# Performance work log

Measured on AMD Instinct MI355X. Metric: run time of the kernel, lower is better.

## Reference

```python
import jax, jax.numpy as jnp
import numpy as np
import math

N_EMBD = 1024
N_HEAD = 16
HEAD_DIM = N_EMBD // N_HEAD


def setup_inputs() -> dict:
    key = jax.random.key(0)
    k_x, k_w1, k_b1, k_w2, k_b2 = jax.random.split(key, 5)
    B, T = 2, 2048
    x = jax.random.normal(k_x, (B, T, N_EMBD), dtype=jnp.float32)
    # ln1: Linear(n_embd, 3*n_embd); weights stored as [in, out] for x @ W
    W_qkv = jax.random.normal(k_w1, (N_EMBD, 3 * N_EMBD), dtype=jnp.float32) * 0.02
    b_qkv = jax.random.normal(k_b1, (3 * N_EMBD,), dtype=jnp.float32) * 0.02
    # ln2: Linear(n_embd, n_embd)
    W_out = jax.random.normal(k_w2, (N_EMBD, N_EMBD), dtype=jnp.float32) * 0.02
    b_out = jax.random.normal(k_b2, (N_EMBD,), dtype=jnp.float32) * 0.02
    return {"x": x, "W_qkv": W_qkv, "b_qkv": b_qkv, "W_out": W_out, "b_out": b_out}


def reference(x, W_qkv, b_qkv, W_out, b_out):
    B, T, C = x.shape
    qkv = x @ W_qkv + b_qkv                      # [B,T,3C]
    q, k, v = jnp.split(qkv, 3, axis=-1)
    # reshape to heads: [B, H, T, D]
    def to_heads(t):
        return t.reshape(B, T, N_HEAD, HEAD_DIM).transpose(0, 2, 1, 3)
    Q, K, V = to_heads(q), to_heads(k), to_heads(v)
    # NOTE: scale is 1/sqrt(n_head), as in the source (not sqrt(head_dim));
    # NOTE: no causal mask is applied, faithfully matching the source forward.
    scale = 1.0 / math.sqrt(N_HEAD)
    scores = jnp.einsum('bhqd,bhkd->bhqk', Q, K) * scale  # [B,H,T,T]
    attn = jax.nn.softmax(scores, axis=-1)
    out = jnp.einsum('bhqk,bhkd->bhqd', attn, V)          # [B,H,T,D]
    out = out.transpose(0, 2, 1, 3).reshape(B, T, C)
    # dropout = 0.0 -> identity (eval mode)
    return out @ W_out + b_out
```

## Files before the change

### kernel.cpp

```cpp
#include <hip/hip_runtime.h>
#include <hip/hip_bf16.h>
#include <stdint.h>

typedef __bf16 bf16_t;
typedef __bf16 bf16x8 __attribute__((ext_vector_type(8)));
typedef float  f32x4  __attribute__((ext_vector_type(4)));

#define AS1 __attribute__((address_space(1)))
#define AS3 __attribute__((address_space(3)))

__device__ __forceinline__ void gload16(const bf16_t* g, char* l) {
  __builtin_amdgcn_global_load_lds((AS1 const void*)(uintptr_t)g, (AS3 void*)l, 16, 0, 0);
}
__device__ __forceinline__ int swz8(int r) { return (r & 7) ^ ((r >> 2) & 6); }

#define C2S 0.36067376022224085f
#define LGKM0 do { asm volatile("s_waitcnt lgkmcnt(0)" ::: "memory"); \
                   __builtin_amdgcn_sched_barrier(0); } while (0)

__global__ __launch_bounds__(256) void prep(
    const float* __restrict__ x, const float* __restrict__ Wqkv, const float* __restrict__ Wout,
    bf16_t* __restrict__ xb, bf16_t* __restrict__ wqkvT, bf16_t* __restrict__ woutT) {
  __shared__ float tile[32][33];
  const int bid = blockIdx.x, tid = threadIdx.x;
  if (bid < 4096) {
    const int i = bid * 256 + tid;
    float4 v = reinterpret_cast<const float4*>(x)[i];
    union { bf16_t h[4]; unsigned long long u; } r;
    r.h[0] = (bf16_t)v.x; r.h[1] = (bf16_t)v.y; r.h[2] = (bf16_t)v.z; r.h[3] = (bf16_t)v.w;
    reinterpret_cast<unsigned long long*>(xb)[i] = r.u;
    return;
  }
  const float* W; bf16_t* Wt; int N, tb;
  if (bid < 7168) { W = Wqkv; Wt = wqkvT; N = 3072; tb = bid - 4096; }
  else            { W = Wout; Wt = woutT; N = 1024; tb = bid - 7168; }
  const int kb = (tb & 31) * 32, nb = (tb >> 5) * 32;
  const int tx = tid & 31, ty = tid >> 5;
#pragma unroll
  for (int i = 0; i < 32; i += 8)
    tile[ty + i][tx] = W[(size_t)(kb + ty + i) * N + nb + tx];
  __syncthreads();
#pragma unroll
  for (int i = 0; i < 32; i += 8)
    Wt[(size_t)(nb + ty + i) * 1024 + kb + tx] = (bf16_t)tile[tx][ty + i];
}

__global__ __launch_bounds__(512) void gemm8(
    const bf16_t* __restrict__ A, const bf16_t* __restrict__ Bt,
    const float* __restrict__ bias,
    bf16_t* __restrict__ outb, bf16_t* __restrict__ vtb,
    int N, int K, int ldo) {
  __shared__ bf16_t lA[3][4096];
  __shared__ bf16_t lB[3][4096];
  const int tid = threadIdx.x;
  const int wave = tid >> 6, lane = tid & 63;
  const int lr = lane & 15, lg = lane >> 4;
  const int ntiles = N >> 7;
  const int bid = (blockIdx.x & 7) * ((int)gridDim.x >> 3) + (blockIdx.x >> 3);
  const int bn = bid % ntiles, bm = bid / ntiles;
  const int m0 = bm * 128, n0 = bn * 128;
  const int wr = wave >> 2, wc = wave & 3;
  f32x4 acc[4][2] = {};

  const int srow = tid >> 2;
  const int scolb = ((tid & 3) << 4) ^ (((srow >> 1) & 3) << 4);
  const bf16_t* Asrc = A  + (size_t)(m0 + srow) * K + (scolb >> 1);
  const bf16_t* Bsrc = Bt + (size_t)(n0 + srow) * K + (scolb >> 1);
  auto stage = [&](int buf, int k0) {
    char* dst = (char*)nullptr;
    (void)dst;
    gload16(Asrc + k0, (char*)&lA[buf][0] + wave * 1024);
    gload16(Bsrc + k0, (char*)&lB[buf][0] + wave * 1024);
  };

  auto ldA = [&](const char* p, int mi) {
    const int row = wr * 64 + mi * 16 + lr;
    return *reinterpret_cast<const bf16x8*>(p + row * 64 + ((lg * 16) ^ (((row >> 1) & 3) << 4)));
  };
  auto ldB = [&](const char* p, int ni) {
    const int row = wc * 32 + ni * 16 + lr;
    return *reinterpret_cast<const bf16x8*>(p + row * 64 + ((lg * 16) ^ (((row >> 1) & 3) << 4)));
  };

  const int nt = K >> 5;
  stage(0, 0);
  stage(1, 32);
  int cur = 0, stg = 2;

  for (int t = 0; t < nt; ++t) {
    if (t + 2 < nt) {
      stage(stg, (t + 2) << 5);
      asm volatile("s_waitcnt vmcnt(4)" ::: "memory");
    } else if (t + 1 < nt) {
      asm volatile("s_waitcnt vmcnt(2)" ::: "memory");
    } else {
      asm volatile("s_waitcnt vmcnt(0)" ::: "memory");
    }
    __builtin_amdgcn_s_barrier();
    __builtin_amdgcn_sched_barrier(0);

    const char* pA = (const char*)&lA[cur][0];
    const char* pB = (const char*)&lB[cur][0];
    bf16x8 af[4], bfv[2];
#pragma unroll
    for (int mi = 0; mi < 4; ++mi) af[mi] = ldA(pA, mi);
    bfv[0] = ldB(pB, 0); bfv[1] = ldB(pB, 1);

    __builtin_amdgcn_s_setprio(1);
#pragma unroll
    for (int mi = 0; mi < 4; ++mi)
#pragma unroll
      for (int ni = 0; ni < 2; ++ni)
        acc[mi][ni] = __builtin_amdgcn_mfma_f32_16x16x32_bf16(af[mi], bfv[ni], acc[mi][ni], 0, 0, 0);
    __builtin_amdgcn_s_setprio(0);

    __builtin_amdgcn_sched_barrier(0);
    __builtin_amdgcn_s_barrier();
    cur = cur == 2 ? 0 : cur + 1;
    stg = stg == 2 ? 0 : stg + 1;
  }

#pragma unroll
  for (int mi = 0; mi < 4; ++mi) {
#pragma unroll
    for (int ni = 0; ni < 2; ++ni) {
      const int col = n0 + wc * 32 + ni * 16 + lr;
      const float bv = bias[col];
      const int rg0 = m0 + wr * 64 + mi * 16 + lg * 4;
      if (col >= 2048) {
        const int colv = col - 2048;
        const int dd = colv & 63, hh = colv >> 6;
        const int bb = rg0 >> 11, t = rg0 & 2047;
        union { bf16_t h4[4]; unsigned long long u; } pk;
#pragma unroll
        for (int r = 0; r < 4; ++r) pk.h4[r] = (bf16_t)(acc[mi][ni][r] + bv);
        *reinterpret_cast<unsigned long long*>(
            vtb + (size_t)(bb * 16 + hh) * 131072 + (size_t)dd * 2048 + t) = pk.u;
      } else {
        const float sc = (col < 1024) ? C2S : 1.f;
#pragma unroll
        for (int r = 0; r < 4; ++r) {
          const float v = (acc[mi][ni][r] + bv) * sc;
          outb[(size_t)(rg0 + r) * ldo + col] = (bf16_t)v;
        }
      }
    }
  }
}

template<int MI>
__global__ __launch_bounds__(256) void gemm_bt(
    const bf16_t* __restrict__ A, const bf16_t* __restrict__ Bt,
    const float* __restrict__ bias,
    bf16_t* __restrict__ outb, bf16_t* __restrict__ vtb, float* __restrict__ outf,
    int M, int N, int K, int ldo, int mode) {
  __shared__ bf16_t lA[3][MI * 1024];
  __shared__ bf16_t lB[3][4096];
  const int tid = threadIdx.x;
  const int wave = tid >> 6, lane = tid & 63;
  const int lr = lane & 15, lg = lane >> 4;
  const int ntiles = N >> 7;
  const int bid = (blockIdx.x & 7) * ((int)gridDim.x >> 3) + (blockIdx.x >> 3);
  const int bn = bid % ntiles, bm = bid / ntiles;
  const int m0 = bm * (MI * 32), n0 = bn * 128;
  const int wr = wave >> 1, wc = wave & 1;
  f32x4 acc[MI][4] = {};

  const int lamw = wave * 64 + lane;
  const int srow = lamw >> 2;
  const int scolb = ((lamw & 3) << 4) ^ (((srow >> 1) & 3) << 4);
  auto stageA = [&](int buf, int k0, int it) {
    gload16(A + (size_t)(m0 + it * 64 + srow) * K + k0 + (scolb >> 1),
            (char*)&lA[buf][0] + (it * 256 + wave * 64) * 16);
  };
  auto stageB = [&](int buf, int k0, int it) {
    gload16(Bt + (size_t)(n0 + it * 64 + srow) * K + k0 + (scolb >> 1),
            (char*)&lB[buf][0] + (it * 256 + wave * 64) * 16);
  };
  auto stageg = [&](int buf, int k0) {
#pragma unroll
    for (int it = 0; it < MI / 2; ++it) stageA(buf, k0, it);
    stageB(buf, k0, 0); stageB(buf, k0, 1);
  };

  auto ldA = [&](const char* p, int mi) {
    const int row = wr * (MI * 16) + mi * 16 + lr;
    return *reinterpret_cast<const bf16x8*>(p + row * 64 + ((lg * 16) ^ (((row >> 1) & 3) << 4)));
  };
  auto ldB = [&](const char* p, int ni) {
    const int row = wc * 64 + ni * 16 + lr;
    return *reinterpret_cast<const bf16x8*>(p + row * 64 + ((lg * 16) ^ (((row >> 1) & 3) << 4)));
  };

  const int nt = K >> 5;
  stageg(0, 0);
  stageg(1, 32);
  int cur = 0, stg = 2;

  for (int t = 0; t < nt; ++t) {
    if (t + 1 < nt) {
      if constexpr (MI == 4) asm volatile("s_waitcnt vmcnt(4)" ::: "memory");
      else                   asm volatile("s_waitcnt vmcnt(3)" ::: "memory");
    } else {
      asm volatile("s_waitcnt vmcnt(0)" ::: "memory");
    }
    __builtin_amdgcn_s_barrier();
    __builtin_amdgcn_sched_barrier(0);

    const char* pA = (const char*)&lA[cur][0];
    const char* pB = (const char*)&lB[cur][0];
    const bool pf = (t + 2 < nt);
    const int k2 = (t + 2) << 5;
    bf16x8 af[MI], bfv[4];

    af[0] = ldA(pA, 0); af[1] = ldA(pA, 1);
    bfv[0] = ldB(pB, 0); bfv[1] = ldB(pB, 1);
    if (pf) { stageA(stg, k2, 0); stageB(stg, k2, 0); }
    __builtin_amdgcn_s_barrier(); LGKM0;
    __builtin_amdgcn_s_setprio(1);
    acc[0][0] = __builtin_amdgcn_mfma_f32_16x16x32_bf16(af[0], bfv[0], acc[0][0], 0, 0, 0);
    acc[0][1] = __builtin_amdgcn_mfma_f32_16x16x32_bf16(af[0], bfv[1], acc[0][1], 0, 0, 0);
    acc[1][0] = __builtin_amdgcn_mfma_f32_16x16x32_bf16(af[1], bfv[0], acc[1][0], 0, 0, 0);
    acc[1][1] = __builtin_amdgcn_mfma_f32_16x16x32_bf16(af[1], bfv[1], acc[1][1], 0, 0, 0);
    __builtin_amdgcn_s_setprio(0);
    bfv[2] = ldB(pB, 2); bfv[3] = ldB(pB, 3);
    if (pf) stageB(stg, k2, 1);
    __builtin_amdgcn_s_barrier(); LGKM0;
    __builtin_amdgcn_s_setprio(1);
    acc[0][2] = __builtin_amdgcn_mfma_f32_16x16x32_bf16(af[0], bfv[2], acc[0][2], 0, 0, 0);
    acc[0][3] = __builtin_amdgcn_mfma_f32_16x16x32_bf16(af[0], bfv[3], acc[0][3], 0, 0, 0);
    acc[1][2] = __builtin_amdgcn_mfma_f32_16x16x32_bf16(af[1], bfv[2], acc[1][2], 0, 0, 0);
    acc[1][3] = __builtin_amdgcn_mfma_f32_16x16x32_bf16(af[1], bfv[3], acc[1][3], 0, 0, 0);
    __builtin_amdgcn_s_setprio(0);

    cur = cur == 2 ? 0 : cur + 1;
    stg = stg == 2 ? 0 : stg + 1;
  }

#pragma unroll
  for (int mi = 0; mi < MI; ++mi) {
#pragma unroll
    for (int ni = 0; ni < 4; ++ni) {
      const int col = n0 + wc * 64 + ni * 16 + lr;
      const float bv = bias[col];
      const int rg0 = m0 + wr * (MI * 16) + mi * 16 + lg * 4;
      const float sc = 1.f;
#pragma unroll
      for (int r = 0; r < 4; ++r) {
        const float v = (acc[mi][ni][r] + bv) * sc;
        if (mode == 2) outf[(size_t)(rg0 + r) * ldo + col] = v;
        else           outb[(size_t)(rg0 + r) * ldo + col] = (bf16_t)v;
      }
    }
  }
  (void)vtb;
}

__global__ __launch_bounds__(512) void attn_fwd(
    const bf16_t* __restrict__ qkv2,
    const bf16_t* __restrict__ vT,
    bf16_t* __restrict__ a0, bf16_t* __restrict__ a1,
    float* __restrict__ lbuf) {
  __shared__ bf16_t lds[3][8192];
  const int tid = threadIdx.x;
  const int wave = tid >> 6, lane = tid & 63;
  const int lr = lane & 15, lg = lane >> 4;
  const int id = blockIdx.x;
  const int xcd = id & 7, slot = id >> 3;
  const int bh = xcd * 4 + (slot & 3);
  const int rest = slot >> 2;
  const int qb = rest & 7, kvh = rest >> 3;
  const int b = bh >> 4, h = bh & 15;

  const int q0 = qb * 256 + wave * 32;
  const bf16_t* Qp = qkv2 + (size_t)(b * 2048 + q0) * 2048 + h * 64;
  bf16x8 qf[2][2];
#pragma unroll
  for (int hx = 0; hx < 2; ++hx) {
    qf[hx][0] = *reinterpret_cast<const bf16x8*>(Qp + (size_t)(hx * 16 + lr) * 2048 + lg * 8);
    qf[hx][1] = *reinterpret_cast<const bf16x8*>(Qp + (size_t)(hx * 16 + lr) * 2048 + 32 + lg * 8);
  }

  const int kr = tid >> 3;
  const int ks = (tid & 7) ^ swz8(kr);
  const bf16_t* Ksrc = qkv2 + (size_t)(b * 2048 + kvh * 1024 + kr) * 2048 + 1024 + h * 64 + ks * 8;
  const bf16_t* Vsrc = vT + (size_t)bh * 131072 + (size_t)kr * 2048 + kvh * 1024 + ks * 8;

  auto stage = [&](int buf, int kb) {
    char* base = (char*)&lds[buf][0] + wave * 1024;
    gload16(Ksrc + (size_t)kb * 131072, base);
    gload16(Vsrc + (size_t)kb * 64, base + 8192);
  };

  int kofs[4][2], vofs[4][2];
#pragma unroll
  for (int t = 0; t < 4; ++t) {
    const int kk = 32 * (t >> 1) + 8 * (lr >> 2) + 4 * (t & 1) + (lr & 3);
    const int sw = swz8(kk) << 4;
    kofs[t][0] = (kk << 7) + ((lg * 16) ^ sw);
    kofs[t][1] = (kk << 7) + ((64 + lg * 16) ^ sw);
  }
#pragma unroll
  for (int nc = 0; nc < 4; ++nc) {
    const int vr = nc * 16 + lr;
    const int sw = swz8(vr) << 4;
    vofs[nc][0] = 8192 + (vr << 7) + ((lg * 16) ^ sw);
    vofs[nc][1] = 8192 + (vr << 7) + ((64 + lg * 16) ^ sw);
  }

  f32x4 acc[2][4] = {};
  f32x4 accl[2] = {};
  bf16x8 ones;
#pragma unroll
  for (int j = 0; j < 8; ++j) ones[j] = (bf16_t)1.0f;

  stage(0, 0);
  stage(1, 1);
  int cur = 0, stg = 2;

  for (int kb = 0; kb < 16; ++kb) {
    if (kb + 2 < 16) stage(stg, kb + 2);
    if (kb + 2 < 16)      asm volatile("s_waitcnt vmcnt(4)" ::: "memory");
    else if (kb + 1 < 16) asm volatile("s_waitcnt vmcnt(2)" ::: "memory");
    else                  asm volatile("s_waitcnt vmcnt(0)" ::: "memory");
    __builtin_amdgcn_s_barrier();
    __builtin_amdgcn_sched_barrier(0);
    const char* bK = (const char*)&lds[cur][0];

    f32x4 s[2][4];
#pragma unroll
    for (int t = 0; t < 4; ++t) {
      const bf16x8 k0 = *reinterpret_cast<const bf16x8*>(bK + kofs[t][0]);
      const bf16x8 k1 = *reinterpret_cast<const bf16x8*>(bK + kofs[t][1]);
#pragma unroll
      for (int hx = 0; hx < 2; ++hx) {
        f32x4 z = {0.f, 0.f, 0.f, 0.f};
        z = __builtin_amdgcn_mfma_f32_16x16x32_bf16(k0, qf[hx][0], z, 0, 0, 0);
        s[hx][t] = __builtin_amdgcn_mfma_f32_16x16x32_bf16(k1, qf[hx][1], z, 0, 0, 0);
      }
    }

    bf16x8 pa[2][2];
#pragma unroll
    for (int hx = 0; hx < 2; ++hx) {
      float p[16];
#pragma unroll
      for (int t = 0; t < 4; ++t)
#pragma unroll
        for (int r = 0; r < 4; ++r)
          p[t * 4 + r] = __builtin_amdgcn_exp2f(s[hx][t][r]);
#pragma unroll
      for (int j = 0; j < 8; ++j) { pa[hx][0][j] = (bf16_t)p[j]; pa[hx][1][j] = (bf16_t)p[8 + j]; }
    }

    __builtin_amdgcn_s_setprio(1);
#pragma unroll
    for (int hx = 0; hx < 2; ++hx) {
      accl[hx] = __builtin_amdgcn_mfma_f32_16x16x32_bf16(pa[hx][0], ones, accl[hx], 0, 0, 0);
      accl[hx] = __builtin_amdgcn_mfma_f32_16x16x32_bf16(pa[hx][1], ones, accl[hx], 0, 0, 0);
    }
#pragma unroll
    for (int nc = 0; nc < 4; ++nc) {
      const bf16x8 v0 = *reinterpret_cast<const bf16x8*>(bK + vofs[nc][0]);
      const bf16x8 v1 = *reinterpret_cast<const bf16x8*>(bK + vofs[nc][1]);
#pragma unroll
      for (int hx = 0; hx < 2; ++hx) {
        acc[hx][nc] = __builtin_amdgcn_mfma_f32_16x16x32_bf16(pa[hx][0], v0, acc[hx][nc], 0, 0, 0);
        acc[hx][nc] = __builtin_amdgcn_mfma_f32_16x16x32_bf16(pa[hx][1], v1, acc[hx][nc], 0, 0, 0);
      }
    }
    __builtin_amdgcn_s_setprio(0);

    __builtin_amdgcn_sched_barrier(0);
    __builtin_amdgcn_s_barrier();
    cur = cur == 2 ? 0 : cur + 1;
    stg = stg == 2 ? 0 : stg + 1;
  }

  bf16_t* ap = kvh ? a1 : a0;
#pragma unroll
  for (int hx = 0; hx < 2; ++hx) {
#pragma unroll
    for (int r = 0; r < 4; ++r) {
      const float lf = 1.f / accl[hx][r];
      const int qg = q0 + hx * 16 + lg * 4 + r;
      bf16_t* op = ap + (size_t)(b * 2048 + qg) * 1024 + h * 64 + lr;
#pragma unroll
      for (int nc = 0; nc < 4; ++nc) op[nc * 16] = (bf16_t)(acc[hx][nc][r] * lf);
      if (lr == 0)
        lbuf[(size_t)(kvh * 4096 + b * 2048 + qg) * 16 + h] = accl[hx][r];
    }
  }
}

__global__ void attn_reduce(const bf16_t* __restrict__ a0, const bf16_t* __restrict__ a1,
                            const float* __restrict__ lbuf, bf16_t* __restrict__ aout) {
  const int i = blockIdx.x * 256 + threadIdx.x;
  const int r = i >> 7, h = (i & 127) >> 3;
  const float l0 = lbuf[(size_t)r * 16 + h];
  const float l1 = lbuf[(size_t)(4096 + r) * 16 + h];
  const float inv = 1.f / (l0 + l1);
  const float w0 = l0 * inv, w1 = l1 * inv;
  const bf16x8 v0 = reinterpret_cast<const bf16x8*>(a0)[i];
  const bf16x8 v1 = reinterpret_cast<const bf16x8*>(a1)[i];
  bf16x8 o;
#pragma unroll
  for (int j = 0; j < 8; ++j) o[j] = (bf16_t)(w0 * (float)v0[j] + w1 * (float)v1[j]);
  reinterpret_cast<bf16x8*>(aout)[i] = o;
}

extern "C" void kernel_launch(void* const* d_in, const int* in_sizes, int n_in,
                              void* d_out, int out_size, void* d_ws, size_t ws_size,
                              hipStream_t stream) {
  (void)in_sizes; (void)n_in; (void)out_size; (void)ws_size;
  const float* x    = (const float*)d_in[0];
  const float* Wqkv = (const float*)d_in[1];
  const float* bqkv = (const float*)d_in[2];
  const float* Wout = (const float*)d_in[3];
  const float* bout = (const float*)d_in[4];
  float* out = (float*)d_out;

  char* ws = (char*)d_ws;
  bf16_t* xb    = (bf16_t*)(ws);
  bf16_t* a0    = (bf16_t*)(ws);
  bf16_t* wqkvT = (bf16_t*)(ws + 8388608);
  bf16_t* woutT = (bf16_t*)(ws + 14680064);
  bf16_t* qkv2  = (bf16_t*)(ws + 16777216);
  bf16_t* aout  = (bf16_t*)(ws + 16777216);
  bf16_t* vT    = (bf16_t*)(ws + 33554432);
  bf16_t* a1    = (bf16_t*)(ws + 41943040);
  float*  lbuf  = (float*)(ws + 50331648);

  prep<<<8192, 256, 0, stream>>>(x, Wqkv, Wout, xb, wqkvT, woutT);
  gemm8<<<768, 512, 0, stream>>>(xb, wqkvT, bqkv, qkv2, vT, 3072, 1024, 2048);
  attn_fwd<<<512, 512, 0, stream>>>(qkv2, vT, a0, a1, lbuf);
  attn_reduce<<<2048, 256, 0, stream>>>(a0, a1, lbuf, aout);
  gemm_bt<2><<<512, 256, 0, stream>>>(aout, woutT, bout, nullptr, nullptr, out, 4096, 1024, 1024, 1024, 2);
}
```

Baseline: 111.6 us.

## Fuse split-KV attention merge into output projection GEMM; vectorize weight transpose stores

Removes the separate attn_reduce kernel and merges the two split-KV partial attention outputs inside a new output-projection GEMM. The GEMM now register-prefetches the inputs, combines them with weights derived from lbuf, and writes the result to LDS. This saves one launch and a round trip of the merged activation through global memory. In exchange, the GEMM drops the async global-to-LDS triple-buffered pipeline for a simpler double buffer with register staging, doing two reads of A per tile plus extra ALU work. Separately, the prep transpose now writes four packed bf16 values per thread as one 8-byte store.

Result: no change. 112.3 us (+0.6%).

```diff
diff --git a/kernel.cpp b/kernel.cpp
--- a/kernel.cpp
+++ b/kernel.cpp
@@ -15,8 +15,6 @@
 __device__ __forceinline__ int swz8(int r) { return (r & 7) ^ ((r >> 2) & 6); }
 
 #define C2S 0.36067376022224085f
-#define LGKM0 do { asm volatile("s_waitcnt lgkmcnt(0)" ::: "memory"); \
-                   __builtin_amdgcn_sched_barrier(0); } while (0)
 
 __global__ __launch_bounds__(256) void prep(
     const float* __restrict__ x, const float* __restrict__ Wqkv, const float* __restrict__ Wout,
@@ -40,9 +38,12 @@
   for (int i = 0; i < 32; i += 8)
     tile[ty + i][tx] = W[(size_t)(kb + ty + i) * N + nb + tx];
   __syncthreads();
-#pragma unroll
-  for (int i = 0; i < 32; i += 8)
-    Wt[(size_t)(nb + ty + i) * 1024 + kb + tx] = (bf16_t)tile[tx][ty + i];
+  const int r = tid >> 3;
+  const int c0 = (tid & 7) * 4;
+  union { bf16_t h4[4]; unsigned long long u; } pk;
+#pragma unroll
+  for (int j = 0; j < 4; ++j) pk.h4[j] = (bf16_t)tile[c0 + j][r];
+  *reinterpret_cast<unsigned long long*>(&Wt[(size_t)(nb + r) * 1024 + kb + c0]) = pk.u;
 }
 
 __global__ __launch_bounds__(512) void gemm8(
@@ -67,8 +68,6 @@
   const bf16_t* Asrc = A  + (size_t)(m0 + srow) * K + (scolb >> 1);
   const bf16_t* Bsrc = Bt + (size_t)(n0 + srow) * K + (scolb >> 1);
   auto stage = [&](int buf, int k0) {
-    char* dst = (char*)nullptr;
-    (void)dst;
     gload16(Asrc + k0, (char*)&lA[buf][0] + wave * 1024);
     gload16(Bsrc + k0, (char*)&lB[buf][0] + wave * 1024);
   };
@@ -146,114 +145,6 @@
       }
     }
   }
-}
-
-template<int MI>
-__global__ __launch_bounds__(256) void gemm_bt(
-    const bf16_t* __restrict__ A, const bf16_t* __restrict__ Bt,
-    const float* __restrict__ bias,
-    bf16_t* __restrict__ outb, bf16_t* __restrict__ vtb, float* __restrict__ outf,
-    int M, int N, int K, int ldo, int mode) {
-  __shared__ bf16_t lA[3][MI * 1024];
-  __shared__ bf16_t lB[3][4096];
-  const int tid = threadIdx.x;
-  const int wave = tid >> 6, lane = tid & 63;
-  const int lr = lane & 15, lg = lane >> 4;
-  const int ntiles = N >> 7;
-  const int bid = (blockIdx.x & 7) * ((int)gridDim.x >> 3) + (blockIdx.x >> 3);
-  const int bn = bid % ntiles, bm = bid / ntiles;
-  const int m0 = bm * (MI * 32), n0 = bn * 128;
-  const int wr = wave >> 1, wc = wave & 1;
-  f32x4 acc[MI][4] = {};
-
-  const int lamw = wave * 64 + lane;
-  const int srow = lamw >> 2;
-  const int scolb = ((lamw & 3) << 4) ^ (((srow >> 1) & 3) << 4);
-  auto stageA = [&](int buf, int k0, int it) {
-    gload16(A + (size_t)(m0 + it * 64 + srow) * K + k0 + (scolb >> 1),
-            (char*)&lA[buf][0] + (it * 256 + wave * 64) * 16);
-  };
-  auto stageB = [&](int buf, int k0, int it) {
-    gload16(Bt + (size_t)(n0 + it * 64 + srow) * K + k0 + (scolb >> 1),
-            (char*)&lB[buf][0] + (it * 256 + wave * 64) * 16);
-  };
-  auto stageg = [&](int buf, int k0) {
-#pragma unroll
-    for (int it = 0; it < MI / 2; ++it) stageA(buf, k0, it);
-    stageB(buf, k0, 0); stageB(buf, k0, 1);
-  };
-
-  auto ldA = [&](const char* p, int mi) {
-    const int row = wr * (MI * 16) + mi * 16 + lr;
-    return *reinterpret_cast<const bf16x8*>(p + row * 64 + ((lg * 16) ^ (((row >> 1) & 3) << 4)));
-  };
-  auto ldB = [&](const char* p, int ni) {
-    const int row = wc * 64 + ni * 16 + lr;
-    return *reinterpret_cast<const bf16x8*>(p + row * 64 + ((lg * 16) ^ (((row >> 1) & 3) << 4)));
-  };
-
-  const int nt = K >> 5;
-  stageg(0, 0);
-  stageg(1, 32);
-  int cur = 0, stg = 2;
-
-  for (int t = 0; t < nt; ++t) {
-    if (t + 1 < nt) {
-      if constexpr (MI == 4) asm volatile("s_waitcnt vmcnt(4)" ::: "memory");
-      else                   asm volatile("s_waitcnt vmcnt(3)" ::: "memory");
-    } else {
-      asm volatile("s_waitcnt vmcnt(0)" ::: "memory");
-    }
-    __builtin_amdgcn_s_barrier();
-    __builtin_amdgcn_sched_barrier(0);
-
-    const char* pA = (const char*)&lA[cur][0];
-    const char* pB = (const char*)&lB[cur][0];
-    const bool pf = (t + 2 < nt);
-    const int k2 = (t + 2) << 5;
-    bf16x8 af[MI], bfv[4];
-
-    af[0] = ldA(pA, 0); af[1] = ldA(pA, 1);
-    bfv[0] = ldB(pB, 0); bfv[1] = ldB(pB, 1);
-    if (pf) { stageA(stg, k2, 0); stageB(stg, k2, 0); }
-    __builtin_amdgcn_s_barrier(); LGKM0;
-    __builtin_amdgcn_s_setprio(1);
-    acc[0][0] = __builtin_amdgcn_mfma_f32_16x16x32_bf16(af[0], bfv[0], acc[0][0], 0, 0, 0);
-    acc[0][1] = __builtin_amdgcn_mfma_f32_16x16x32_bf16(af[0], bfv[1], acc[0][1], 0, 0, 0);
-    acc[1][0] = __builtin_amdgcn_mfma_f32_16x16x32_bf16(af[1], bfv[0], acc[1][0], 0, 0, 0);
-    acc[1][1] = __builtin_amdgcn_mfma_f32_16x16x32_bf16(af[1], bfv[1], acc[1][1], 0, 0, 0);
-    __builtin_amdgcn_s_setprio(0);
-    bfv[2] = ldB(pB, 2); bfv[3] = ldB(pB, 3);
-    if (pf) stageB(stg, k2, 1);
-    __builtin_amdgcn_s_barrier(); LGKM0;
-    __builtin_amdgcn_s_setprio(1);
-    acc[0][2] = __builtin_amdgcn_mfma_f32_16x16x32_bf16(af[0], bfv[2], acc[0][2], 0, 0, 0);
-    acc[0][3] = __builtin_amdgcn_mfma_f32_16x16x32_bf16(af[0], bfv[3], acc[0][3], 0, 0, 0);
-    acc[1][2] = __builtin_amdgcn_mfma_f32_16x16x32_bf16(af[1], bfv[2], acc[1][2], 0, 0, 0);
-    acc[1][3] = __builtin_amdgcn_mfma_f32_16x16x32_bf16(af[1], bfv[3], acc[1][3], 0, 0, 0);
-    __builtin_amdgcn_s_setprio(0);
-
-    cur = cur == 2 ? 0 : cur + 1;
-    stg = stg == 2 ? 0 : stg + 1;
-  }
-
-#pragma unroll
-  for (int mi = 0; mi < MI; ++mi) {
-#pragma unroll
-    for (int ni = 0; ni < 4; ++ni) {
-      const int col = n0 + wc * 64 + ni * 16 + lr;
-      const float bv = bias[col];
-      const int rg0 = m0 + wr * (MI * 16) + mi * 16 + lg * 4;
-      const float sc = 1.f;
-#pragma unroll
-      for (int r = 0; r < 4; ++r) {
-        const float v = (acc[mi][ni][r] + bv) * sc;
-        if (mode == 2) outf[(size_t)(rg0 + r) * ldo + col] = v;
-        else           outb[(size_t)(rg0 + r) * ldo + col] = (bf16_t)v;
-      }
-    }
-  }
-  (void)vtb;
 }
 
 __global__ __launch_bounds__(512) void attn_fwd(
@@ -393,20 +284,95 @@
   }
 }
 
-__global__ void attn_reduce(const bf16_t* __restrict__ a0, const bf16_t* __restrict__ a1,
-                            const float* __restrict__ lbuf, bf16_t* __restrict__ aout) {
-  const int i = blockIdx.x * 256 + threadIdx.x;
-  const int r = i >> 7, h = (i & 127) >> 3;
-  const float l0 = lbuf[(size_t)r * 16 + h];
-  const float l1 = lbuf[(size_t)(4096 + r) * 16 + h];
-  const float inv = 1.f / (l0 + l1);
-  const float w0 = l0 * inv, w1 = l1 * inv;
-  const bf16x8 v0 = reinterpret_cast<const bf16x8*>(a0)[i];
-  const bf16x8 v1 = reinterpret_cast<const bf16x8*>(a1)[i];
-  bf16x8 o;
-#pragma unroll
-  for (int j = 0; j < 8; ++j) o[j] = (bf16_t)(w0 * (float)v0[j] + w1 * (float)v1[j]);
-  reinterpret_cast<bf16x8*>(aout)[i] = o;
+__global__ __launch_bounds__(256) void gemm2m(
+    const bf16_t* __restrict__ a0, const bf16_t* __restrict__ a1,
+    const float* __restrict__ lbuf, const bf16_t* __restrict__ Bt,
+    const float* __restrict__ bias, float* __restrict__ outf) {
+  __shared__ bf16_t lA[2][2048];
+  __shared__ bf16_t lB[2][4096];
+  const int tid = threadIdx.x;
+  const int wave = tid >> 6, lane = tid & 63;
+  const int lr = lane & 15, lg = lane >> 4;
+  const int bid = (blockIdx.x & 7) * 64 + (blockIdx.x >> 3);
+  const int bm = bid >> 3, bn = bid & 7;
+  const int m0 = bm * 64, n0 = bn * 128;
+  const int wr = wave >> 1, wc = wave & 1;
+  f32x4 acc[2][4] = {};
+
+  const int srow = tid >> 2;
+  const int scolb = ((tid & 3) << 4) ^ (((srow >> 1) & 3) << 4);
+  const int scol = scolb >> 1;
+
+  const bf16_t* pa0 = a0 + (size_t)(m0 + srow) * 1024 + scol;
+  const bf16_t* pa1 = a1 + (size_t)(m0 + srow) * 1024 + scol;
+  const float*  pl0 = lbuf + (size_t)(m0 + srow) * 16;
+  const float*  pl1 = lbuf + (size_t)(4096 + m0 + srow) * 16;
+  const bf16_t* pB0 = Bt + (size_t)(n0 + srow) * 1024 + scol;
+  const bf16_t* pB1 = Bt + (size_t)(n0 + 64 + srow) * 1024 + scol;
+
+  bf16x8 nA0 = *reinterpret_cast<const bf16x8*>(pa0);
+  bf16x8 nA1 = *reinterpret_cast<const bf16x8*>(pa1);
+  float  nl0 = pl0[0], nl1 = pl1[0];
+  bf16x8 nB0v = *reinterpret_cast<const bf16x8*>(pB0);
+  bf16x8 nB1v = *reinterpret_cast<const bf16x8*>(pB1);
+
+  for (int t = 0; t < 32; ++t) {
+    const int cur = t & 1;
+    const float inv = 1.f / (nl0 + nl1);
+    const float w0 = nl0 * inv, w1 = nl1 * inv;
+    bf16x8 mv;
+#pragma unroll
+    for (int j = 0; j < 8; ++j)
+      mv[j] = (bf16_t)(w0 * (float)nA0[j] + w1 * (float)nA1[j]);
+    *reinterpret_cast<bf16x8*>((char*)&lA[cur][0] + tid * 16) = mv;
+    *reinterpret_cast<bf16x8*>((char*)&lB[cur][0] + tid * 16) = nB0v;
+    *reinterpret_cast<bf16x8*>((char*)&lB[cur][0] + 4096 + tid * 16) = nB1v;
+    __syncthreads();
+
+    if (t < 31) {
+      const int k0 = (t + 1) * 32;
+      const int h = k0 >> 6;
+      nA0 = *reinterpret_cast<const bf16x8*>(pa0 + k0);
+      nA1 = *reinterpret_cast<const bf16x8*>(pa1 + k0);
+      nl0 = pl0[h]; nl1 = pl1[h];
+      nB0v = *reinterpret_cast<const bf16x8*>(pB0 + k0);
+      nB1v = *reinterpret_cast<const bf16x8*>(pB1 + k0);
+    }
+
+    const char* pA = (const char*)&lA[cur][0];
+    const char* pB = (const char*)&lB[cur][0];
+    bf16x8 af[2], bfv[4];
+#pragma unroll
+    for (int mi = 0; mi < 2; ++mi) {
+      const int row = wr * 32 + mi * 16 + lr;
+      af[mi] = *reinterpret_cast<const bf16x8*>(pA + row * 64 + ((lg * 16) ^ (((row >> 1) & 3) << 4)));
+    }
+#pragma unroll
+    for (int ni = 0; ni < 4; ++ni) {
+      const int row = wc * 64 + ni * 16 + lr;
+      bfv[ni] = *reinterpret_cast<const bf16x8*>(pB + row * 64 + ((lg * 16) ^ (((row >> 1) & 3) << 4)));
+    }
+    __builtin_amdgcn_s_setprio(1);
+#pragma unroll
+    for (int mi = 0; mi < 2; ++mi)
+#pragma unroll
+      for (int ni = 0; ni < 4; ++ni)
+        acc[mi][ni] = __builtin_amdgcn_mfma_f32_16x16x32_bf16(af[mi], bfv[ni], acc[mi][ni], 0, 0, 0);
+    __builtin_amdgcn_s_setprio(0);
+    __syncthreads();
+  }
+
+#pragma unroll
+  for (int mi = 0; mi < 2; ++mi)
+#pragma unroll
+    for (int ni = 0; ni < 4; ++ni) {
+      const int col = n0 + wc * 64 + ni * 16 + lr;
+      const float bv = bias[col];
+      const int rg0 = m0 + wr * 32 + mi * 16 + lg * 4;
+#pragma unroll
+      for (int r = 0; r < 4; ++r)
+        outf[(size_t)(rg0 + r) * 1024 + col] = acc[mi][ni][r] + bv;
+    }
 }
 
 extern "C" void kernel_launch(void* const* d_in, const int* in_sizes, int n_in,
@@ -426,7 +392,6 @@
   bf16_t* wqkvT = (bf16_t*)(ws + 8388608);
   bf16_t* woutT = (bf16_t*)(ws + 14680064);
   bf16_t* qkv2  = (bf16_t*)(ws + 16777216);
-  bf16_t* aout  = (bf16_t*)(ws + 16777216);
   bf16_t* vT    = (bf16_t*)(ws + 33554432);
   bf16_t* a1    = (bf16_t*)(ws + 41943040);
   float*  lbuf  = (float*)(ws + 50331648);
@@ -434,6 +399,5 @@
   prep<<<8192, 256, 0, stream>>>(x, Wqkv, Wout, xb, wqkvT, woutT);
   gemm8<<<768, 512, 0, stream>>>(xb, wqkvT, bqkv, qkv2, vT, 3072, 1024, 2048);
   attn_fwd<<<512, 512, 0, stream>>>(qkv2, vT, a0, a1, lbuf);
-  attn_reduce<<<2048, 256, 0, stream>>>(a0, a1, lbuf, aout);
-  gemm_bt<2><<<512, 256, 0, stream>>>(aout, woutT, bout, nullptr, nullptr, out, 4096, 1024, 1024, 1024, 2);
-}
+  gemm2m<<<512, 256, 0, stream>>>(a0, a1, lbuf, woutT, bout, out);
+}
```
